# Performance work log

Measured on AMD Instinct MI355X. Metric: run time of the kernel, lower is better.

## Reference

```python
import jax, jax.numpy as jnp
import numpy as np

NMS_THR = 0.5
SCORE_THR = 0.05
MAX_BOXES = 300
N_ANCHORS = 5000
N_CLASSES = 80
IMG = 640.0  # image size used to scale synthetic box coords


def setup_inputs() -> dict:
    key = jax.random.key(0)
    k1, k2, k3 = jax.random.split(key, 3)
    # build well-formed boxes (x1<=x2, y1<=y2) in a 640x640 image
    c1 = jax.random.uniform(k1, (1, N_ANCHORS, 2), jnp.float32) * IMG
    c2 = jax.random.uniform(k2, (1, N_ANCHORS, 2), jnp.float32) * IMG
    boxes = jnp.concatenate([jnp.minimum(c1, c2), jnp.maximum(c1, c2) + 1.0], axis=-1)
    # classification scores in [0,1], squared to skew toward low values like sigmoid logits
    classification = jax.random.uniform(k3, (1, N_ANCHORS, N_CLASSES), jnp.float32) ** 2
    return {"boxes": boxes, "classification": classification}


def _iou_matrix(b):
    # b: [N,4] as (x1,y1,x2,y2) -> [N,N] pairwise IoU
    x1, y1, x2, y2 = b[:, 0], b[:, 1], b[:, 2], b[:, 3]
    area = (x2 - x1) * (y2 - y1)
    iw = jnp.maximum(jnp.minimum(x2[:, None], x2[None, :]) - jnp.maximum(x1[:, None], x1[None, :]), 0.0)
    ih = jnp.maximum(jnp.minimum(y2[:, None], y2[None, :]) - jnp.maximum(y1[:, None], y1[None, :]), 0.0)
    inter = iw * ih
    union = area[:, None] + area[None, :] - inter
    return inter / jnp.maximum(union, 1e-8)


def _nms_one_class(scores, iou):
    # greedy NMS for one class; scores: [N], iou: [N,N] (shared across classes)
    n = scores.shape[0]
    order = jnp.argsort(-scores)          # descending score order
    valid = scores > SCORE_THR            # per-class score-threshold filter
    idxs = jnp.arange(n)

    def step(carry, oi):
        suppressed, kept, count = carry
        alive = (~suppressed[oi]) & valid[oi] & (count < MAX_BOXES)
        # a kept box suppresses all others with IoU above threshold
        suppressed = suppressed | (alive & (iou[oi] > NMS_THR) & (idxs != oi))
        kept = kept.at[oi].set(alive)
        return (suppressed, kept, count + alive.astype(jnp.int32)), None

    init = (jnp.zeros(n, jnp.bool_), jnp.zeros(n, jnp.bool_), jnp.int32(0))
    (_, kept, _), _ = jax.lax.scan(step, init, order)
    return kept  # [N] bool mask in original index space


def reference(boxes, classification):
    b = boxes[0]             # [N,4]
    cls = classification[0]  # [N,C]
    iou = _iou_matrix(b)     # [N,N], class-independent
    kept = jax.vmap(_nms_one_class, in_axes=(1, None))(cls, iou)  # [C,N]
    # scatter surviving scores back to dense per-class score map (zeros elsewhere)
    selected = jnp.where(kept.T, cls, 0.0)                        # [N,C]
    detections = jnp.concatenate([b, selected], axis=1)           # [N,4+C]
    return detections[None]                                       # [1,N,4+C]
```

## Files before the change

### kernel.cpp

```cpp
#include <hip/hip_runtime.h>

#define N_ANCHORS 5000
#define N_CLASSES 80
#define OUT_COLS  84
#define MAX_BOXES 300
#define SCORE_THR 0.05f

#define SORT_PAD  5056
#define NB        4096
#define BLOCK     1024
#define SLOTS     8
#define DONEP     0x40000000

typedef unsigned long long u64;
typedef unsigned int u32;

#define WG __HIP_MEMORY_SCOPE_WORKGROUP

__device__ __forceinline__ float readlane_f(float v, int l) {
    return __int_as_float(__builtin_amdgcn_readlane(__float_as_int(v), l));
}
__device__ __forceinline__ u32 aload(u32* p) {
    return __hip_atomic_load(p, __ATOMIC_ACQUIRE, WG);
}
__device__ __forceinline__ int bucket_of(float s) {
    float u = sqrtf(s);
    int b = (int)((u - 0.2236f) * 5275.0f);
    return min(max(b, 0), NB - 1);
}
__device__ __forceinline__ bool iou_q(float4 a, float aa, float4 q) {
    float iw = fmaxf(fminf(a.z, q.z) - fmaxf(a.x, q.x), 0.0f);
    float ih = fmaxf(fminf(a.w, q.w) - fmaxf(a.y, q.y), 0.0f);
    float aq = (q.z - q.x) * (q.w - q.y);
    return 3.0f * (iw * ih) > aa + aq;
}

#define INIT_BLKS 1641
#define TR_BX     157
#define TR_BY     3
#define TR_BLKS   (TR_BX * TR_BY)

__global__ __launch_bounds__(256) void prep(const float* __restrict__ boxes,
                                            const float* __restrict__ cls,
                                            float* __restrict__ clsT,
                                            float* __restrict__ out) {
    __shared__ float tile[32][33];
    int b = blockIdx.x;
    if (b < INIT_BLKS) {
        int i = b * 256 + threadIdx.x;
        if (i < N_ANCHORS * OUT_COLS) {
            int row = i / OUT_COLS, col = i - row * OUT_COLS;
            out[i] = (col < 4) ? boxes[row * 4 + col] : 0.0f;
        }
        return;
    }
    b -= INIT_BLKS;
    int bx_ = b % TR_BX, by_ = b / TR_BX;
    int j0 = bx_ * 32, c0 = by_ * 32;
    int tx = threadIdx.x & 31, ty = threadIdx.x >> 5;
    #pragma unroll
    for (int r = 0; r < 32; r += 8) {
        int j = j0 + ty + r, c = c0 + tx;
        tile[ty + r][tx] = (j < N_ANCHORS && c < N_CLASSES) ? cls[j * N_CLASSES + c] : 0.0f;
    }
    __syncthreads();
    #pragma unroll
    for (int r = 0; r < 32; r += 8) {
        int c = c0 + ty + r, j = j0 + tx;
        if (c < N_CLASSES && j < N_ANCHORS) clsT[(size_t)c * N_ANCHORS + j] = tile[tx][ty + r];
    }
}

__global__ __launch_bounds__(BLOCK, 1) void nms(const float* __restrict__ clsT,
                                                const float4* __restrict__ boxes4,
                                                float* __restrict__ out) {
    __shared__ __align__(16) char SMEM[62016];
    u64*    lk    = (u64*)SMEM;
    u32*    hist  = (u32*)(SMEM + 40448);
    u64*    Iring = (u64*)(SMEM + 40448);
    float4* Bring = (float4*)(SMEM + 44544);
    u64*    kout  = (u64*)(SMEM + 52736);
    float4* kbox  = (float4*)(SMEM + 56832);
    u64*    KS    = (u64*)(SMEM + 61760);
    u32*    wtot  = (u32*)(SMEM + 61824);
    u32*    KBa   = (u32*)(SMEM + 61888);
    u32*    flagI = (u32*)(SMEM + 61920);
    u32*    flagK = (u32*)(SMEM + 61952);
    u32*    prog  = (u32*)(SMEM + 61984);
    u32*    kcnt  = (u32*)(SMEM + 61988);

    const int c = blockIdx.x;
    const int t = threadIdx.x;
    const int lane = t & 63;
    const int wv = t >> 6;

    const float4* cp4 = (const float4*)(clsT + (size_t)c * N_ANCHORS);
    u32 sb[8];
    #pragma unroll
    for (int m = 0; m < 2; ++m) {
        int vi = m * 1024 + t;
        float4 v = make_float4(0.f, 0.f, 0.f, 0.f);
        if (vi < N_ANCHORS / 4) v = cp4[vi];
        sb[m * 4 + 0] = (v.x > SCORE_THR) ? __float_as_uint(v.x) : 0u;
        sb[m * 4 + 1] = (v.y > SCORE_THR) ? __float_as_uint(v.y) : 0u;
        sb[m * 4 + 2] = (v.z > SCORE_THR) ? __float_as_uint(v.z) : 0u;
        sb[m * 4 + 3] = (v.w > SCORE_THR) ? __float_as_uint(v.w) : 0u;
    }
    for (int b = t; b < NB; b += BLOCK) hist[b] = 0u;
    if (t < 308) kbox[t] = make_float4(1e9f, 1e9f, 1e9f, 1e9f);
    if (t < SLOTS) { flagI[t] = 0u; flagK[t] = 0u; }
    if (t == 0) { *prog = 0u; *kcnt = 0u; }
    __syncthreads();
    #pragma unroll
    for (int m = 0; m < 8; ++m)
        if (sb[m]) atomicAdd(&hist[bucket_of(__uint_as_float(sb[m]))], 1u);
    __syncthreads();

    const int hbase = t * 4;
    u32 vals[4]; u32 run = 0;
    #pragma unroll
    for (int k = 0; k < 4; ++k) { run += hist[hbase + k]; vals[k] = run; }
    u32 x = run;
    #pragma unroll
    for (int off = 1; off < 64; off <<= 1) { u32 y = __shfl_up(x, off); if (lane >= off) x += y; }
    if (lane == 63) wtot[wv] = x;
    __syncthreads();
    u32 woff = 0;
    for (int w = 0; w < wv; ++w) woff += wtot[w];
    const u32 exb = woff + x - run;
    #pragma unroll
    for (int k = 0; k < 4; ++k) hist[hbase + k] = exb + (k ? vals[k - 1] : 0u);
    __syncthreads();
    #pragma unroll
    for (int m = 0; m < 8; ++m) {
        if (sb[m]) {
            int j = ((m >> 2) * 1024 + t) * 4 + (m & 3);
            u32 pos = atomicAdd(&hist[bucket_of(__uint_as_float(sb[m]))], 1u);
            lk[pos] = ((u64)sb[m] << 32) | (u32)(~(u32)j);
        }
    }
    __syncthreads();
    const int total = (int)hist[NB - 1];
    for (int v = total + t; v < SORT_PAD; v += BLOCK) lk[v] = 0ull;
    for (int b = hbase; b < hbase + 4; ++b) {
        int s0 = b ? (int)hist[b - 1] : 0;
        int e  = (int)hist[b];
        for (int i = s0 + 1; i < e; ++i) {
            u64 key = lk[i]; int q = i - 1;
            while (q >= s0 && lk[q] < key) { lk[q + 1] = lk[q]; --q; }
            lk[q + 1] = key;
        }
    }
    __syncthreads();
    const int nch = (total + 63) >> 6;

    if (wv >= 1 && wv <= 4) {
        for (int j = wv - 1; j < nch; j += 4) {
            const int slot = j & (SLOTS - 1);
            u64 e = lk[j * 64 + lane];
            u32 jj = e ? ~(u32)e : 0u;
            float4 bx = boxes4[jj];
            float ar = (bx.z - bx.x) * (bx.w - bx.y);
            u32 p;
            for (;;) {
                p = aload(prog);
                if ((int)p >= j - (SLOTS - 1)) break;
                __builtin_amdgcn_s_sleep(2);
            }
            if (p >= DONEP) return;
            u64 word = 0ull;
            #pragma unroll 16
            for (int q = 0; q < 64; ++q) {
                float4 o;
                o.x = readlane_f(bx.x, q); o.y = readlane_f(bx.y, q);
                o.z = readlane_f(bx.z, q); o.w = readlane_f(bx.w, q);
                if (iou_q(bx, ar, o)) word |= (1ull << q);
            }
            Iring[slot * 64 + lane] = word;
            if (lane == 0)
                __hip_atomic_store(&flagI[slot], (u32)(j + 1), __ATOMIC_RELEASE, WG);
        }
        return;
    }
    if (wv >= 5) {
        for (int j = wv - 5; j < nch; j += 11) {
            const int slot = j & (SLOTS - 1);
            u64 e = lk[j * 64 + lane];
            bool validL = (e != 0ull);
            u32 jj = validL ? ~(u32)e : 0u;
            float4 bx = boxes4[jj];
            float ar = (bx.z - bx.x) * (bx.w - bx.y);
            u32 p;
            for (;;) {
                p = aload(prog);
                if ((int)p >= j - (SLOTS - 1)) break;
                __builtin_amdgcn_s_sleep(2);
            }
            if (p >= DONEP) return;
            Bring[slot * 64 + lane] = bx;
            bool sup = !validL;
            u32 ka = aload(kcnt);
            u32 kaR = (ka + 7) & ~7u;
            for (u32 r = 0; r < kaR; r += 8) {
                float4 q0 = kbox[r + 0], q1 = kbox[r + 1], q2 = kbox[r + 2], q3 = kbox[r + 3];
                float4 q4 = kbox[r + 4], q5 = kbox[r + 5], q6 = kbox[r + 6], q7 = kbox[r + 7];
                bool s = iou_q(bx, ar, q0) | iou_q(bx, ar, q1) | iou_q(bx, ar, q2) | iou_q(bx, ar, q3)
                       | iou_q(bx, ar, q4) | iou_q(bx, ar, q5) | iou_q(bx, ar, q6) | iou_q(bx, ar, q7);
                sup = sup || s;
                if (__ballot(!sup) == 0ull) break;
            }
            for (;;) {
                p = aload(prog);
                if ((int)p >= j - 2) break;
                __builtin_amdgcn_s_sleep(1);
            }
            u32 kb2 = (p >= DONEP) ? ka : aload(kcnt);
            if (kb2 < ka) kb2 = ka;
            u32 r1 = (kb2 + 3) & ~3u;
            for (u32 r = ka & ~3u; r < r1; r += 4) {
                float4 q0 = kbox[r + 0], q1 = kbox[r + 1], q2 = kbox[r + 2], q3 = kbox[r + 3];
                bool s = iou_q(bx, ar, q0) | iou_q(bx, ar, q1) | iou_q(bx, ar, q2) | iou_q(bx, ar, q3);
                sup = sup || s;
            }
            u64 ks = __ballot(sup);
            if (lane == 0) {
                KS[slot] = ks; KBa[slot] = kb2;
                __hip_atomic_store(&flagK[slot], (u32)(j + 1), __ATOMIC_RELEASE, WG);
            }
            if (p >= DONEP) return;
        }
        return;
    }

    int kept = 0; u32 kcur = 0; bool capped = false;
    for (int k = 0; k < nch; ++k) {
        const int slot = k & (SLOTS - 1);
        u64 key = lk[k * 64 + lane];
        bool valid = (key != 0ull);
        u32 j = valid ? ~(u32)key : 0u;
        float sc = __uint_as_float((u32)(key >> 32));

        while (aload(&flagK[slot]) != (u32)(k + 1)) { }
        u64 ks = KS[slot];
        if (ks != ~0ull) {
            u32 kb = KBa[slot];
            float4 bx = Bring[slot * 64 + lane];
            float ar = (bx.z - bx.x) * (bx.w - bx.y);
            bool alive = valid && !((ks >> lane) & 1ull);
            u32 r1 = (kcur + 3) & ~3u;
            for (u32 r = kb & ~3u; r < r1; r += 4) {
                float4 q0 = kbox[r + 0], q1 = kbox[r + 1], q2 = kbox[r + 2], q3 = kbox[r + 3];
                bool s = iou_q(bx, ar, q0) | iou_q(bx, ar, q1) | iou_q(bx, ar, q2) | iou_q(bx, ar, q3);
                alive = alive && !s;
            }
            u64 rem = __ballot(alive);
            if (rem) {
                while (aload(&flagI[slot]) != (u32)(k + 1)) { }
                u64 I = Iring[slot * 64 + lane];
                u64 km = 0ull;
                while (rem) {
                    int pos = __ffsll((long long)rem) - 1;
                    km |= 1ull << pos;
                    if (++kept == MAX_BOXES) { capped = true; break; }
                    u32 lo = (u32)__builtin_amdgcn_readlane((int)(u32)I, pos);
                    u32 hi = (u32)__builtin_amdgcn_readlane((int)(u32)(I >> 32), pos);
                    rem &= ~(((u64)hi << 32) | (u64)lo);
                }
                if ((km >> lane) & 1ull) {
                    int rank = (int)__popcll(km & ((1ull << lane) - 1ull));
                    kbox[kcur + rank] = bx;
                    kout[kcur + rank] = ((u64)__float_as_uint(sc) << 32) | j;
                }
                kcur += (u32)__popcll(km);
            }
        }
        if (capped) break;
        if (lane == 0) {
            __hip_atomic_store(kcnt, kcur, __ATOMIC_RELEASE, WG);
            __hip_atomic_store(prog, (u32)(k + 1), __ATOMIC_RELEASE, WG);
        }
    }
    if (lane == 0) __hip_atomic_store(prog, (u32)DONEP, __ATOMIC_RELEASE, WG);

    for (u32 i = (u32)lane; i < kcur; i += 64) {
        u64 e = kout[i];
        out[(size_t)((u32)e) * OUT_COLS + 4 + c] = __uint_as_float((u32)(e >> 32));
    }
}

extern "C" void kernel_launch(void* const* d_in, const int* in_sizes, int n_in,
                              void* d_out, int out_size, void* d_ws, size_t ws_size,
                              hipStream_t stream) {
    const float* boxes = (const float*)d_in[0];
    const float* cls   = (const float*)d_in[1];
    float* out = (float*)d_out;
    float* clsT = (float*)d_ws;

    prep<<<INIT_BLKS + TR_BLKS, 256, 0, stream>>>(boxes, cls, clsT, out);
    nms<<<N_CLASSES, BLOCK, 0, stream>>>(clsT, (const float4*)boxes, out);
}
```

Measured before the change: 142.0 us.

## Transpose prefilter IoU loop: lanes hold kept boxes, iterate candidates via readlane

The prefilter helper waves used to have each lane test its own candidate box against every kept box, reading the kept boxes from shared memory in groups of eight. Now each lane holds up to five kept boxes in registers. The wave loops over the valid candidates, broadcasts each one with readlane, and uses a ballot for an early-exit per candidate. This swaps repeated LDS reads for register-resident data and lane-parallel checks, but adds a serial 64-step loop with ballots per chunk. The kbox padding grows to 320 entries so that five full 64-wide groups can be loaded.

```diff
diff --git a/kernel.cpp b/kernel.cpp
--- a/kernel.cpp
+++ b/kernel.cpp
@@ -74,20 +74,20 @@
 __global__ __launch_bounds__(BLOCK, 1) void nms(const float* __restrict__ clsT,
                                                 const float4* __restrict__ boxes4,
                                                 float* __restrict__ out) {
-    __shared__ __align__(16) char SMEM[62016];
+    __shared__ __align__(16) char SMEM[62208];
     u64*    lk    = (u64*)SMEM;
     u32*    hist  = (u32*)(SMEM + 40448);
     u64*    Iring = (u64*)(SMEM + 40448);
     float4* Bring = (float4*)(SMEM + 44544);
     u64*    kout  = (u64*)(SMEM + 52736);
     float4* kbox  = (float4*)(SMEM + 56832);
-    u64*    KS    = (u64*)(SMEM + 61760);
-    u32*    wtot  = (u32*)(SMEM + 61824);
-    u32*    KBa   = (u32*)(SMEM + 61888);
-    u32*    flagI = (u32*)(SMEM + 61920);
-    u32*    flagK = (u32*)(SMEM + 61952);
-    u32*    prog  = (u32*)(SMEM + 61984);
-    u32*    kcnt  = (u32*)(SMEM + 61988);
+    u64*    KS    = (u64*)(SMEM + 61952);
+    u32*    wtot  = (u32*)(SMEM + 62016);
+    u32*    KBa   = (u32*)(SMEM + 62080);
+    u32*    flagI = (u32*)(SMEM + 62112);
+    u32*    flagK = (u32*)(SMEM + 62144);
+    u32*    prog  = (u32*)(SMEM + 62176);
+    u32*    kcnt  = (u32*)(SMEM + 62180);
 
     const int c = blockIdx.x;
     const int t = threadIdx.x;
@@ -107,7 +107,7 @@
         sb[m * 4 + 3] = (v.w > SCORE_THR) ? __float_as_uint(v.w) : 0u;
     }
     for (int b = t; b < NB; b += BLOCK) hist[b] = 0u;
-    if (t < 308) kbox[t] = make_float4(1e9f, 1e9f, 1e9f, 1e9f);
+    if (t < 320) kbox[t] = make_float4(1e9f, 1e9f, 1e9f, 1e9f);
     if (t < SLOTS) { flagI[t] = 0u; flagK[t] = 0u; }
     if (t == 0) { *prog = 0u; *kcnt = 0u; }
     __syncthreads();
@@ -198,17 +198,38 @@
             }
             if (p >= DONEP) return;
             Bring[slot * 64 + lane] = bx;
-            bool sup = !validL;
+            u64 vm = __ballot(validL);
+            u64 ks = ~vm;
             u32 ka = aload(kcnt);
-            u32 kaR = (ka + 7) & ~7u;
-            for (u32 r = 0; r < kaR; r += 8) {
-                float4 q0 = kbox[r + 0], q1 = kbox[r + 1], q2 = kbox[r + 2], q3 = kbox[r + 3];
-                float4 q4 = kbox[r + 4], q5 = kbox[r + 5], q6 = kbox[r + 6], q7 = kbox[r + 7];
-                bool s = iou_q(bx, ar, q0) | iou_q(bx, ar, q1) | iou_q(bx, ar, q2) | iou_q(bx, ar, q3)
-                       | iou_q(bx, ar, q4) | iou_q(bx, ar, q5) | iou_q(bx, ar, q6) | iou_q(bx, ar, q7);
-                sup = sup || s;
-                if (__ballot(!sup) == 0ull) break;
-            }
+            const int ng = (int)((ka + 63) >> 6);
+
+            if (ka) {
+                float4 kb[5];
+                #pragma unroll
+                for (int g = 0; g < 5; ++g)
+                    kb[g] = (g < ng) ? kbox[g * 64 + lane]
+                                     : make_float4(1e9f, 1e9f, 1e9f, 1e9f);
+                for (int i = 0; i < 64; ++i) {
+                    if (!((vm >> i) & 1ull)) continue;
+                    float cx1 = readlane_f(bx.x, i), cy1 = readlane_f(bx.y, i);
+                    float cx2 = readlane_f(bx.z, i), cy2 = readlane_f(bx.w, i);
+                    float car = (cx2 - cx1) * (cy2 - cy1);
+                    bool found = false;
+                    #pragma unroll
+                    for (int g = 0; g < 5; ++g) {
+                        if (!found && g < ng) {
+                            float iw = fmaxf(fminf(cx2, kb[g].z) - fmaxf(cx1, kb[g].x), 0.0f);
+                            float ih = fmaxf(fminf(cy2, kb[g].w) - fmaxf(cy1, kb[g].y), 0.0f);
+                            float aq = (kb[g].z - kb[g].x) * (kb[g].w - kb[g].y);
+                            bool s = 3.0f * (iw * ih) > car + aq;
+                            found = (__ballot(s) != 0ull);
+                        }
+                    }
+                    if (found) ks |= (1ull << i);
+                }
+            }
+            bool sup = (ks >> lane) & 1ull;
+
             for (;;) {
                 p = aload(prog);
                 if ((int)p >= j - 2) break;
@@ -222,9 +243,9 @@
                 bool s = iou_q(bx, ar, q0) | iou_q(bx, ar, q1) | iou_q(bx, ar, q2) | iou_q(bx, ar, q3);
                 sup = sup || s;
             }
-            u64 ks = __ballot(sup);
+            u64 ksf = __ballot(sup);
             if (lane == 0) {
-                KS[slot] = ks; KBa[slot] = kb2;
+                KS[slot] = ksf; KBa[slot] = kb2;
                 __hip_atomic_store(&flagK[slot], (u32)(j + 1), __ATOMIC_RELEASE, WG);
             }
             if (p >= DONEP) return;
```

New measurement: 139.9 us. About the same (-1.4%).

## Drop transpose pass, read strided scores directly, simplify helper-wave catch-up check

Applied to the files above, without the earlier changes.

Removes the transpose from the prep kernel so the NMS kernel reads each class's scores directly with strided loads from the original layout. Helper waves no longer wait for near-current progress to re-check newly kept boxes. The main wave now does that catch-up itself, with an 8-wide unrolled loop and padded kbox initialisation. This shortens prep and the helpers' second wait, but the main wave's serial critical path takes on more IoU checks, and the strided score loads are uncoalesced.

```diff
diff --git a/kernel.cpp b/kernel.cpp
--- a/kernel.cpp
+++ b/kernel.cpp
@@ -36,83 +36,56 @@
 }
 
 #define INIT_BLKS 1641
-#define TR_BX     157
-#define TR_BY     3
-#define TR_BLKS   (TR_BX * TR_BY)
 
 __global__ __launch_bounds__(256) void prep(const float* __restrict__ boxes,
-                                            const float* __restrict__ cls,
-                                            float* __restrict__ clsT,
                                             float* __restrict__ out) {
-    __shared__ float tile[32][33];
-    int b = blockIdx.x;
-    if (b < INIT_BLKS) {
-        int i = b * 256 + threadIdx.x;
-        if (i < N_ANCHORS * OUT_COLS) {
-            int row = i / OUT_COLS, col = i - row * OUT_COLS;
-            out[i] = (col < 4) ? boxes[row * 4 + col] : 0.0f;
-        }
-        return;
-    }
-    b -= INIT_BLKS;
-    int bx_ = b % TR_BX, by_ = b / TR_BX;
-    int j0 = bx_ * 32, c0 = by_ * 32;
-    int tx = threadIdx.x & 31, ty = threadIdx.x >> 5;
-    #pragma unroll
-    for (int r = 0; r < 32; r += 8) {
-        int j = j0 + ty + r, c = c0 + tx;
-        tile[ty + r][tx] = (j < N_ANCHORS && c < N_CLASSES) ? cls[j * N_CLASSES + c] : 0.0f;
-    }
-    __syncthreads();
-    #pragma unroll
-    for (int r = 0; r < 32; r += 8) {
-        int c = c0 + ty + r, j = j0 + tx;
-        if (c < N_CLASSES && j < N_ANCHORS) clsT[(size_t)c * N_ANCHORS + j] = tile[tx][ty + r];
-    }
-}
-
-__global__ __launch_bounds__(BLOCK, 1) void nms(const float* __restrict__ clsT,
+    int i = blockIdx.x * 256 + threadIdx.x;
+    if (i < N_ANCHORS * OUT_COLS) {
+        int row = i / OUT_COLS, col = i - row * OUT_COLS;
+        out[i] = (col < 4) ? boxes[row * 4 + col] : 0.0f;
+    }
+}
+
+__global__ __launch_bounds__(BLOCK, 1) void nms(const float* __restrict__ cls,
                                                 const float4* __restrict__ boxes4,
                                                 float* __restrict__ out) {
-    __shared__ __align__(16) char SMEM[62016];
+    __shared__ __align__(16) char SMEM[62208];
     u64*    lk    = (u64*)SMEM;
     u32*    hist  = (u32*)(SMEM + 40448);
     u64*    Iring = (u64*)(SMEM + 40448);
     float4* Bring = (float4*)(SMEM + 44544);
     u64*    kout  = (u64*)(SMEM + 52736);
     float4* kbox  = (float4*)(SMEM + 56832);
-    u64*    KS    = (u64*)(SMEM + 61760);
-    u32*    wtot  = (u32*)(SMEM + 61824);
-    u32*    KBa   = (u32*)(SMEM + 61888);
-    u32*    flagI = (u32*)(SMEM + 61920);
-    u32*    flagK = (u32*)(SMEM + 61952);
-    u32*    prog  = (u32*)(SMEM + 61984);
-    u32*    kcnt  = (u32*)(SMEM + 61988);
+    u64*    KS    = (u64*)(SMEM + 61952);
+    u32*    wtot  = (u32*)(SMEM + 62016);
+    u32*    KBa   = (u32*)(SMEM + 62080);
+    u32*    flagI = (u32*)(SMEM + 62112);
+    u32*    flagK = (u32*)(SMEM + 62144);
+    u32*    prog  = (u32*)(SMEM + 62176);
+    u32*    kcnt  = (u32*)(SMEM + 62180);
 
     const int c = blockIdx.x;
     const int t = threadIdx.x;
     const int lane = t & 63;
     const int wv = t >> 6;
 
-    const float4* cp4 = (const float4*)(clsT + (size_t)c * N_ANCHORS);
-    u32 sb[8];
-    #pragma unroll
-    for (int m = 0; m < 2; ++m) {
-        int vi = m * 1024 + t;
-        float4 v = make_float4(0.f, 0.f, 0.f, 0.f);
-        if (vi < N_ANCHORS / 4) v = cp4[vi];
-        sb[m * 4 + 0] = (v.x > SCORE_THR) ? __float_as_uint(v.x) : 0u;
-        sb[m * 4 + 1] = (v.y > SCORE_THR) ? __float_as_uint(v.y) : 0u;
-        sb[m * 4 + 2] = (v.z > SCORE_THR) ? __float_as_uint(v.z) : 0u;
-        sb[m * 4 + 3] = (v.w > SCORE_THR) ? __float_as_uint(v.w) : 0u;
+    u32 sb[5];
+    #pragma unroll
+    for (int m = 0; m < 5; ++m) {
+        int j = t + m * BLOCK;
+        sb[m] = 0u;
+        if (j < N_ANCHORS) {
+            float s = cls[(size_t)j * N_CLASSES + c];
+            if (s > SCORE_THR) sb[m] = __float_as_uint(s);
+        }
     }
     for (int b = t; b < NB; b += BLOCK) hist[b] = 0u;
-    if (t < 308) kbox[t] = make_float4(1e9f, 1e9f, 1e9f, 1e9f);
+    if (t < 320) kbox[t] = make_float4(1e9f, 1e9f, 1e9f, 1e9f);
     if (t < SLOTS) { flagI[t] = 0u; flagK[t] = 0u; }
     if (t == 0) { *prog = 0u; *kcnt = 0u; }
     __syncthreads();
     #pragma unroll
-    for (int m = 0; m < 8; ++m)
+    for (int m = 0; m < 5; ++m)
         if (sb[m]) atomicAdd(&hist[bucket_of(__uint_as_float(sb[m]))], 1u);
     __syncthreads();
 
@@ -132,9 +105,9 @@
     for (int k = 0; k < 4; ++k) hist[hbase + k] = exb + (k ? vals[k - 1] : 0u);
     __syncthreads();
     #pragma unroll
-    for (int m = 0; m < 8; ++m) {
+    for (int m = 0; m < 5; ++m) {
         if (sb[m]) {
-            int j = ((m >> 2) * 1024 + t) * 4 + (m & 3);
+            int j = t + m * BLOCK;
             u32 pos = atomicAdd(&hist[bucket_of(__uint_as_float(sb[m]))], 1u);
             lk[pos] = ((u64)sb[m] << 32) | (u32)(~(u32)j);
         }
@@ -209,25 +182,11 @@
                 sup = sup || s;
                 if (__ballot(!sup) == 0ull) break;
             }
-            for (;;) {
-                p = aload(prog);
-                if ((int)p >= j - 2) break;
-                __builtin_amdgcn_s_sleep(1);
-            }
-            u32 kb2 = (p >= DONEP) ? ka : aload(kcnt);
-            if (kb2 < ka) kb2 = ka;
-            u32 r1 = (kb2 + 3) & ~3u;
-            for (u32 r = ka & ~3u; r < r1; r += 4) {
-                float4 q0 = kbox[r + 0], q1 = kbox[r + 1], q2 = kbox[r + 2], q3 = kbox[r + 3];
-                bool s = iou_q(bx, ar, q0) | iou_q(bx, ar, q1) | iou_q(bx, ar, q2) | iou_q(bx, ar, q3);
-                sup = sup || s;
-            }
             u64 ks = __ballot(sup);
             if (lane == 0) {
-                KS[slot] = ks; KBa[slot] = kb2;
+                KS[slot] = ks; KBa[slot] = ka;
                 __hip_atomic_store(&flagK[slot], (u32)(j + 1), __ATOMIC_RELEASE, WG);
             }
-            if (p >= DONEP) return;
         }
         return;
     }
@@ -242,15 +201,18 @@
 
         while (aload(&flagK[slot]) != (u32)(k + 1)) { }
         u64 ks = KS[slot];
-        if (ks != ~0ull) {
-            u32 kb = KBa[slot];
+        u32 kb = KBa[slot];
+        bool anyTop = (kb < kcur);
+        if (ks != ~0ull || anyTop) {
             float4 bx = Bring[slot * 64 + lane];
             float ar = (bx.z - bx.x) * (bx.w - bx.y);
             bool alive = valid && !((ks >> lane) & 1ull);
-            u32 r1 = (kcur + 3) & ~3u;
-            for (u32 r = kb & ~3u; r < r1; r += 4) {
+            u32 r1 = (kcur + 7) & ~7u;
+            for (u32 r = kb & ~7u; r < r1; r += 8) {
                 float4 q0 = kbox[r + 0], q1 = kbox[r + 1], q2 = kbox[r + 2], q3 = kbox[r + 3];
-                bool s = iou_q(bx, ar, q0) | iou_q(bx, ar, q1) | iou_q(bx, ar, q2) | iou_q(bx, ar, q3);
+                float4 q4 = kbox[r + 4], q5 = kbox[r + 5], q6 = kbox[r + 6], q7 = kbox[r + 7];
+                bool s = iou_q(bx, ar, q0) | iou_q(bx, ar, q1) | iou_q(bx, ar, q2) | iou_q(bx, ar, q3)
+                       | iou_q(bx, ar, q4) | iou_q(bx, ar, q5) | iou_q(bx, ar, q6) | iou_q(bx, ar, q7);
                 alive = alive && !s;
             }
             u64 rem = __ballot(alive);
@@ -294,8 +256,7 @@
     const float* boxes = (const float*)d_in[0];
     const float* cls   = (const float*)d_in[1];
     float* out = (float*)d_out;
-    float* clsT = (float*)d_ws;
-
-    prep<<<INIT_BLKS + TR_BLKS, 256, 0, stream>>>(boxes, cls, clsT, out);
-    nms<<<N_CLASSES, BLOCK, 0, stream>>>(clsT, (const float4*)boxes, out);
-}
+
+    prep<<<INIT_BLKS, 256, 0, stream>>>(boxes, out);
+    nms<<<N_CLASSES, BLOCK, 0, stream>>>(cls, (const float4*)boxes, out);
+}
```

Result: slower. 170.6 us (+20.1%).
